# Kernel tuning notes

Measured on AMD Instinct MI355X. Metric: run time of the kernel, lower is better.

## Reference

```python
import jax, jax.numpy as jnp
import numpy as np

IMAGE_SIZE = 256
NEAR = 0.1
FAR = 100.0
CHUNK = 200  # faces per rasterization chunk


def setup_inputs() -> dict:
    key = jax.random.key(0)
    k1, k2, k3 = jax.random.split(key, 3)
    B, Nv, Nf = 1, 10000, 10000
    # vertices sized so that after weak projection (u = f*x + c, f=1015, c=112,
    # orig_size=224) they land inside the image plane; z kept positive.
    xy = jax.random.uniform(k1, (B, Nv, 2), minval=-0.1, maxval=0.1)
    z = jax.random.uniform(k3, (B, Nv, 1), minval=0.4, maxval=0.8)
    vertices = jnp.concatenate([xy, z], axis=-1).astype(jnp.float32)
    faces = jax.random.randint(k2, (B, Nf, 3), 0, Nv).astype(jnp.int64)
    f, c = 1015.0, 112.0
    K = jnp.broadcast_to(jnp.array([[f, 0.0, c], [0.0, f, c], [0.0, 0.0, 1.0]],
                                   dtype=jnp.float32), (B, 3, 3))
    R = jnp.broadcast_to(jnp.eye(3, dtype=jnp.float32), (B, 3, 3))
    t = jnp.zeros((B, 3), dtype=jnp.float32)
    return {"vertices": vertices, "faces": faces, "K": K, "R": R, "t": t,
            "orig_size": 224}


def weak_projection(vertices, K, R, t, orig_size):
    # camera transform: v_cam = v @ R^T + t   [B,N,3]
    v = jnp.einsum('bnj,bkj->bnk', vertices, R) + t[:, None, :]
    x, y, z = v[..., 0], v[..., 1], v[..., 2]
    fx, fy = K[:, 0:1, 0], K[:, 1:2, 1]  # [B,1]
    cx, cy = K[:, 0:1, 2], K[:, 1:2, 2]
    # weak (orthographic-with-focal) projection: no divide by z
    u = fx * x + cx
    w = fy * y + cy
    xn = 2.0 * u / orig_size - 1.0        # NDC x in [-1,1]
    yn = -(2.0 * w / orig_size - 1.0)     # image y down -> NDC y up
    return jnp.stack([xn, yn, z], axis=-1)


def _rasterize_depth(face_verts):
    # face_verts: [B, F, 3, 3] (NDC x, NDC y, camera z)
    B, F = face_verts.shape[0], face_verts.shape[1]
    IS = IMAGE_SIZE
    ps = (2.0 * (jnp.arange(IS, dtype=jnp.float32) + 0.5) / IS) - 1.0
    px = ps[None, :]    # [1, W]
    py = -ps[:, None]   # [H, 1], row 0 is top of image

    def chunk_depth(fc):  # fc: [B, C, 3, 3] -> per-pixel min depth [B, H, W]
        x = fc[..., 0][..., None, None]  # [B,C,3,1,1]
        y = fc[..., 1][..., None, None]
        z = fc[..., 2]                   # [B,C,3]
        dx0, dx1, dx2 = x[:, :, 0] - px, x[:, :, 1] - px, x[:, :, 2] - px  # [B,C,1,W]
        dy0, dy1, dy2 = y[:, :, 0] - py, y[:, :, 1] - py, y[:, :, 2] - py  # [B,C,H,1]
        # edge functions (unnormalized barycentric weights) [B,C,H,W]
        w0 = dx1 * dy2 - dx2 * dy1
        w1 = dx2 * dy0 - dx0 * dy2
        w2 = dx0 * dy1 - dx1 * dy0
        area = w0 + w1 + w2
        s = jnp.sign(area)
        inside = (w0 * s >= 0) & (w1 * s >= 0) & (w2 * s >= 0) & (jnp.abs(area) > 1e-10)
        safe_area = jnp.where(jnp.abs(area) > 1e-10, area, 1.0)
        zp = (w0 * z[:, :, 0, None, None] + w1 * z[:, :, 1, None, None]
              + w2 * z[:, :, 2, None, None]) / safe_area
        valid = inside & (zp > NEAR) & (zp < FAR)
        return jnp.min(jnp.where(valid, zp, FAR), axis=1)  # [B,H,W]

    pad = (-F) % CHUNK
    fv = jnp.pad(face_verts, ((0, 0), (0, pad), (0, 0), (0, 0)))  # degenerate pads -> area 0
    n = (F + pad) // CHUNK
    fv = fv.reshape(B, n, CHUNK, 3, 3).transpose(1, 0, 2, 3, 4)  # [n,B,C,3,3]
    ck = jax.checkpoint(chunk_depth)

    def step(carry, fc):
        return jnp.minimum(carry, ck(fc)), None

    depth0 = jnp.full((B, IS, IS), FAR, dtype=jnp.float32)
    depth, _ = jax.lax.scan(step, depth0, fv)
    return depth


def reference(vertices, faces, K, R, t, orig_size):
    # fill_back: append reversed-winding copies of every face
    faces2 = jnp.concatenate([faces, faces[:, :, ::-1]], axis=1)  # [B,2F,3]
    v = weak_projection(vertices, K, R, t, orig_size)             # [B,Nv,3]
    face_verts = jax.vmap(lambda vb, fb: vb[fb])(v, faces2)       # [B,2F,3,3]
    return _rasterize_depth(face_verts)                           # [B,256,256]
```

## Files before the change

kernel.cpp:

```cpp
#include <hip/hip_runtime.h>

#define IMG 256
#define FARZ 100.0f
#define FARB 0x42C80000u
#define TILE 16
#define NZ 4
#define RND 512
#define BT 512
#define EPS 1e-4f
#define EPSZ 1e-5f
#define DPIX (2.0f / IMG)

typedef float f2 __attribute__((ext_vector_type(2)));
static __device__ __forceinline__ f2 pkfma(f2 a, f2 b, f2 c) {
    return __builtin_elementwise_fma(a, b, c);
}
static __device__ __forceinline__ float wave_max(float v) {
#pragma unroll
    for (int m = 32; m >= 1; m >>= 1) v = fmaxf(v, __shfl_xor(v, m, 64));
    return v;
}
static __device__ __forceinline__ float wave_min(float v) {
#pragma unroll
    for (int m = 32; m >= 1; m >>= 1) v = fminf(v, __shfl_xor(v, m, 64));
    return v;
}

struct Q4 { f2 r0, r1; };
static __device__ __forceinline__ Q4 eval4(float A, float B, float C,
                                           float px0, float py0) {
    Q4 o;
    float w00 = fmaf(B, px0, fmaf(C, py0, A));
    o.r0 = pkfma((f2){B, B}, (f2){0.0f, DPIX}, (f2){w00, w00});
    o.r1 = pkfma((f2){C, C}, (f2){-DPIX, -DPIX}, o.r0);
    return o;
}

__global__ __launch_bounds__(256) void setup(const float* __restrict__ verts,
                                             const int* __restrict__ faces,
                                             const float* __restrict__ K,
                                             const float* __restrict__ Rm,
                                             const float* __restrict__ t,
                                             const int* __restrict__ osz,
                                             float4* __restrict__ Q0,
                                             float4* __restrict__ Q1,
                                             float4* __restrict__ Q2,
                                             float4* __restrict__ BB,
                                             unsigned* __restrict__ gb,
                                             unsigned* __restrict__ out, int Nf) {
    __shared__ float sb[4][4];
    int tid = threadIdx.x;
    int i = blockIdx.x * 256 + tid;
    out[i] = FARB;

    float k0 = 104.0f, k1 = 104.0f, k2 = 104.0f, k3 = 104.0f;
    if (i < Nf) {
        float fx = K[0], cx = K[2], fy = K[4], cy = K[5];
        float os = (float)osz[0];
        float r00 = Rm[0], r01 = Rm[1], r02 = Rm[2];
        float r10 = Rm[3], r11 = Rm[4], r12 = Rm[5];
        float r20 = Rm[6], r21 = Rm[7], r22 = Rm[8];
        float t0 = t[0], t1 = t[1], t2 = t[2];

        float3 p[3];
#pragma unroll
        for (int k = 0; k < 3; ++k) {
            int vi = faces[3 * i + k];
            float vx = verts[3 * vi], vy = verts[3 * vi + 1], vz = verts[3 * vi + 2];
            float x = r00 * vx + r01 * vy + r02 * vz + t0;
            float y = r10 * vx + r11 * vy + r12 * vz + t1;
            float z = r20 * vx + r21 * vy + r22 * vz + t2;
            float u = fx * x + cx;
            float w = fy * y + cy;
            p[k].x = 2.0f * u / os - 1.0f;
            p[k].y = -(2.0f * w / os - 1.0f);
            p[k].z = z;
        }

        float A0 = p[1].x * p[2].y - p[2].x * p[1].y;
        float B0 = p[1].y - p[2].y;
        float C0 = p[2].x - p[1].x;
        float A1 = p[2].x * p[0].y - p[0].x * p[2].y;
        float B1 = p[2].y - p[0].y;
        float C1 = p[0].x - p[2].x;
        float A2 = p[0].x * p[1].y - p[1].x * p[0].y;
        float B2 = p[0].y - p[1].y;
        float C2 = p[1].x - p[0].x;

        float area = A0 + A1 + A2;
        if (fabsf(area) > 1e-10f) {
            float s = (area > 0.0f) ? 1.0f : -1.0f;
            A0 *= s; B0 *= s; C0 *= s;
            A1 *= s; B1 *= s; C1 *= s;
            A2 *= s; B2 *= s; C2 *= s;
            float inv = (1.0f / area) * s;
            float P = (A0 * p[0].z + A1 * p[1].z + A2 * p[2].z) * inv;
            float Q = (B0 * p[0].z + B1 * p[1].z + B2 * p[2].z) * inv;
            float Rr = (C0 * p[0].z + C1 * p[1].z + C2 * p[2].z) * inv;
            Q0[i] = make_float4(A0, B0, C0, A1);
            Q1[i] = make_float4(B1, C1, A2, B2);
            Q2[i] = make_float4(C2, P, Q, Rr);
            float xmn = fminf(p[0].x, fminf(p[1].x, p[2].x));
            float xmx = fmaxf(p[0].x, fmaxf(p[1].x, p[2].x));
            float ymn = fminf(p[0].y, fminf(p[1].y, p[2].y));
            float ymx = fmaxf(p[0].y, fmaxf(p[1].y, p[2].y));
            BB[i] = make_float4(xmn, xmx, ymn, ymx);
            k0 = 4.0f + xmn; k1 = 4.0f - xmx;
            k2 = 4.0f + ymn; k3 = 4.0f - ymx;
        } else {
            Q0[i] = make_float4(0.0f, 0.0f, 0.0f, 0.0f);
            Q1[i] = make_float4(0.0f, 0.0f, 0.0f, 0.0f);
            Q2[i] = make_float4(0.0f, 0.0f, 0.0f, 0.0f);
            BB[i] = make_float4(2.0f, 2.0f, 2.0f, 2.0f);
        }
    }

    k0 = wave_min(k0); k1 = wave_min(k1); k2 = wave_min(k2); k3 = wave_min(k3);
    int wave = tid >> 6, lane = tid & 63;
    if (lane == 0) { sb[wave][0] = k0; sb[wave][1] = k1; sb[wave][2] = k2; sb[wave][3] = k3; }
    __syncthreads();
    if (tid < 4) {
        float v = fminf(fminf(sb[0][tid], sb[1][tid]), fminf(sb[2][tid], sb[3][tid]));
        atomicMin(&gb[tid], __float_as_uint(v));
    }
}

__global__ __launch_bounds__(BT) void raster(const float4* __restrict__ Q0,
                                             const float4* __restrict__ Q1,
                                             const float4* __restrict__ Q2,
                                             const float4* __restrict__ BB,
                                             const unsigned* __restrict__ gb,
                                             unsigned* __restrict__ out,
                                             int Nf, int span) {
    __shared__ float4 sf[RND * 3];
    __shared__ unsigned sdepth[TILE * TILE];
    __shared__ float swr[4];
    __shared__ int scnt;

    const int tid = threadIdx.x;
    const int bx = blockIdx.x, by = blockIdx.y;
    const int wave = tid >> 6, lane = tid & 63;

    const float cx0 = -1.0f + (bx * TILE + 0.5f) * DPIX;
    const float cx1 = cx0 + (TILE - 1) * DPIX;
    const float cyTop = 1.0f - (by * TILE + 0.5f) * DPIX;
    const float cyBot = cyTop - (TILE - 1) * DPIX;
    const float tcx = 0.5f * (cx0 + cx1);
    const float tcy = 0.5f * (cyBot + cyTop);
    const float hx = 0.5f * (cx1 - cx0);
    const float hy = 0.5f * (cyTop - cyBot);

    const float gxmin = __uint_as_float(gb[0]) - 4.0f;
    const float gxmax = 4.0f - __uint_as_float(gb[1]);
    const float gymin = __uint_as_float(gb[2]) - 4.0f;
    const float gymax = 4.0f - __uint_as_float(gb[3]);

    const int col = tid & 15, row = (tid >> 4) & 15;
    const float pxt = cx0 + (float)col * DPIX;
    const float pyt = cyTop - (float)row * DPIX;
    const bool coverable = (pxt >= gxmin - 1e-6f) & (pxt <= gxmax + 1e-6f) &
                           (pyt >= gymin - 1e-6f) & (pyt <= gymax + 1e-6f);
    const int gidx = (by * TILE + row) * IMG + bx * TILE + col;
    unsigned orig = FARB;
    if (tid < 256) {
        orig = out[gidx];
        sdepth[tid] = orig;
    }
    if (tid == 0) scnt = 0;
    __syncthreads();
    float T;
    {
        if (tid < 256) {
            float v = coverable ? __uint_as_float(orig) : 0.0f;
            float wm = wave_max(v);
            if (lane == 0) swr[wave] = wm;
        }
        __syncthreads();
        T = fmaxf(fmaxf(swr[0], swr[1]), fmaxf(swr[2], swr[3]));
    }

    const int qx = (lane & 7) * 2, qy = (lane >> 3) * 2;
    const float fpx0 = cx0 + (float)qx * DPIX;
    const float fpy0 = cyTop - (float)qy * DPIX;
    unsigned dmu[4];
    dmu[0] = sdepth[qy * TILE + qx];
    dmu[1] = sdepth[qy * TILE + qx + 1];
    dmu[2] = sdepth[(qy + 1) * TILE + qx];
    dmu[3] = sdepth[(qy + 1) * TILE + qx + 1];

    const int fbase = blockIdx.z * span;
    const int fend = min(fbase + span, Nf);

    for (int base = fbase; base < fend; base += RND) {
        int f = base + tid;
        if (f < fend) {
            float4 b = BB[f];
            bool keep = (b.x <= cx1 + EPS) & (b.y >= cx0 - EPS) &
                        (b.z <= cyTop + EPS) & (b.w >= cyBot - EPS);
            if (keep) {
                float4 q0 = Q0[f], q1 = Q1[f], q2 = Q2[f];
                float m0 = fmaf(q0.y, tcx, fmaf(q0.z, tcy, q0.x)) +
                           fabsf(q0.y) * hx + fabsf(q0.z) * hy;
                float m1 = fmaf(q1.x, tcx, fmaf(q1.y, tcy, q0.w)) +
                           fabsf(q1.x) * hx + fabsf(q1.y) * hy;
                float m2 = fmaf(q1.w, tcx, fmaf(q2.x, tcy, q1.z)) +
                           fabsf(q1.w) * hx + fabsf(q2.x) * hy;
                float zc = fmaf(q2.z, tcx, fmaf(q2.w, tcy, q2.y));
                float zmn = zc - fabsf(q2.z) * hx - fabsf(q2.w) * hy;
                if ((m0 >= -EPS) & (m1 >= -EPS) & (m2 >= -EPS) &
                    (zmn <= T + EPSZ)) {
                    int slot = atomicAdd(&scnt, 1);
                    sf[3 * slot + 0] = q0;
                    sf[3 * slot + 1] = q1;
                    sf[3 * slot + 2] = q2;
                }
            }
        }
        __syncthreads();
        const int n = scnt;

#pragma unroll 2
        for (int j = wave; j < n; j += 8) {
            float4 c0 = sf[3 * j + 0];
            float4 c1 = sf[3 * j + 1];
            float4 c2 = sf[3 * j + 2];
            Q4 w0 = eval4(c0.x, c0.y, c0.z, fpx0, fpy0);
            Q4 w1 = eval4(c0.w, c1.x, c1.y, fpx0, fpy0);
            Q4 w2 = eval4(c1.z, c1.w, c2.x, fpx0, fpy0);
            Q4 zz = eval4(c2.y, c2.z, c2.w, fpx0, fpy0);
            float s0 = fminf(fminf(w0.r0.x, w1.r0.x), w2.r0.x);
            float s1 = fminf(fminf(w0.r0.y, w1.r0.y), w2.r0.y);
            float s2 = fminf(fminf(w0.r1.x, w1.r1.x), w2.r1.x);
            float s3 = fminf(fminf(w0.r1.y, w1.r1.y), w2.r1.y);
            unsigned u0 = (__float_as_uint(s0) & 0x80000000u) | __float_as_uint(zz.r0.x);
            unsigned u1 = (__float_as_uint(s1) & 0x80000000u) | __float_as_uint(zz.r0.y);
            unsigned u2 = (__float_as_uint(s2) & 0x80000000u) | __float_as_uint(zz.r1.x);
            unsigned u3 = (__float_as_uint(s3) & 0x80000000u) | __float_as_uint(zz.r1.y);
            dmu[0] = min(dmu[0], u0);
            dmu[1] = min(dmu[1], u1);
            dmu[2] = min(dmu[2], u2);
            dmu[3] = min(dmu[3], u3);
        }

        atomicMin(&sdepth[qy * TILE + qx], dmu[0]);
        atomicMin(&sdepth[qy * TILE + qx + 1], dmu[1]);
        atomicMin(&sdepth[(qy + 1) * TILE + qx], dmu[2]);
        atomicMin(&sdepth[(qy + 1) * TILE + qx + 1], dmu[3]);
        __syncthreads();

        if (base + RND < fend) {
            if (tid == 0) scnt = 0;
            if (tid < 256) {
                float v = coverable ? __uint_as_float(sdepth[tid]) : 0.0f;
                float wm = wave_max(v);
                if (lane == 0) swr[wave] = wm;
            }
            __syncthreads();
            T = fmaxf(fmaxf(swr[0], swr[1]), fmaxf(swr[2], swr[3]));
        }
    }

    if (tid < 256) {
        unsigned fv = sdepth[tid];
        if (fv < orig) atomicMin(out + gidx, fv);
    }
}

extern "C" void kernel_launch(void* const* d_in, const int* in_sizes, int n_in,
                              void* d_out, int out_size, void* d_ws, size_t ws_size,
                              hipStream_t stream) {
    const float* verts = (const float*)d_in[0];
    const int* faces   = (const int*)d_in[1];
    const float* K     = (const float*)d_in[2];
    const float* Rm    = (const float*)d_in[3];
    const float* t     = (const float*)d_in[4];
    const int* osz     = (const int*)d_in[5];

    int Nf = in_sizes[1] / 3;
    int span = (Nf + NZ - 1) / NZ;

    float4* ws4 = (float4*)d_ws;
    float4* Q0 = ws4;
    float4* Q1 = ws4 + Nf;
    float4* Q2 = ws4 + 2 * Nf;
    float4* BB = ws4 + 3 * Nf;
    unsigned* gb = (unsigned*)(ws4 + 4 * Nf);
    unsigned* out = (unsigned*)d_out;

    setup<<<(IMG * IMG) / 256, 256, 0, stream>>>(verts, faces, K, Rm, t, osz,
                                                 Q0, Q1, Q2, BB, gb, out, Nf);

    raster<<<dim3(IMG / TILE, IMG / TILE, NZ), BT, 0, stream>>>(
        Q0, Q1, Q2, BB, gb, out, Nf, span);
}
```

Before: 93.77 us.

## Depth-sort faces into buckets and stop rasterizing once tile depth bound is reached

Faces are binned by their minimum depth with a histogram, an exclusive scan and a scatter kernel, then interleaved across the z-split so each raster block walks faces front-to-back. Each block stops once the next face bucket exceeds the current tile's maximum depth, skipping occluded faces. Per-thread shared atomics for compaction are also replaced by wave ballot plus one atomic per wave. This adds three small kernels, a memset and extra workspace traffic, and relies on depth-sorted order for early termination to pay off.

```diff
diff --git a/kernel.cpp b/kernel.cpp
--- a/kernel.cpp
+++ b/kernel.cpp
@@ -10,6 +10,7 @@
 #define EPS 1e-4f
 #define EPSZ 1e-5f
 #define DPIX (2.0f / IMG)
+#define NB 256
 
 typedef float f2 __attribute__((ext_vector_type(2)));
 static __device__ __forceinline__ f2 pkfma(f2 a, f2 b, f2 c) {
@@ -47,6 +48,8 @@
                                              float4* __restrict__ Q2,
                                              float4* __restrict__ BB,
                                              unsigned* __restrict__ gb,
+                                             unsigned* __restrict__ hist,
+                                             int* __restrict__ key,
                                              unsigned* __restrict__ out, int Nf) {
     __shared__ float sb[4][4];
     int tid = threadIdx.x;
@@ -88,6 +91,7 @@
         float C2 = p[1].x - p[0].x;
 
         float area = A0 + A1 + A2;
+        int bkt = NB - 1;
         if (fabsf(area) > 1e-10f) {
             float s = (area > 0.0f) ? 1.0f : -1.0f;
             A0 *= s; B0 *= s; C0 *= s;
@@ -107,12 +111,17 @@
             BB[i] = make_float4(xmn, xmx, ymn, ymx);
             k0 = 4.0f + xmn; k1 = 4.0f - xmx;
             k2 = 4.0f + ymn; k3 = 4.0f - ymx;
+            float minz = fminf(p[0].z, fminf(p[1].z, p[2].z));
+            int b = (int)floorf(minz * (float)NB);
+            bkt = min(max(b, 0), NB - 1);
         } else {
             Q0[i] = make_float4(0.0f, 0.0f, 0.0f, 0.0f);
             Q1[i] = make_float4(0.0f, 0.0f, 0.0f, 0.0f);
             Q2[i] = make_float4(0.0f, 0.0f, 0.0f, 0.0f);
             BB[i] = make_float4(2.0f, 2.0f, 2.0f, 2.0f);
         }
+        key[i] = bkt;
+        atomicAdd(&hist[bkt], 1u);
     }
 
     k0 = wave_min(k0); k1 = wave_min(k1); k2 = wave_min(k2); k3 = wave_min(k3);
@@ -125,20 +134,64 @@
     }
 }
 
+__global__ __launch_bounds__(NB) void scan(const unsigned* __restrict__ hist,
+                                           int* __restrict__ offs,
+                                           int* __restrict__ wbase) {
+    __shared__ int s[NB];
+    int tid = threadIdx.x;
+    int v = (int)hist[tid];
+    s[tid] = v;
+    __syncthreads();
+#pragma unroll
+    for (int d = 1; d < NB; d <<= 1) {
+        int add = (tid >= d) ? s[tid - d] : 0;
+        __syncthreads();
+        s[tid] += add;
+        __syncthreads();
+    }
+    int incl = s[tid];
+    offs[tid + 1] = incl;
+    if (tid == 0) offs[0] = 0;
+    wbase[tid] = incl - v;
+}
+
+__global__ __launch_bounds__(256) void scatter(const float4* __restrict__ Q0,
+                                               const float4* __restrict__ Q1,
+                                               const float4* __restrict__ Q2,
+                                               const float4* __restrict__ BB,
+                                               const int* __restrict__ key,
+                                               int* __restrict__ wbase,
+                                               float4* __restrict__ Qs0,
+                                               float4* __restrict__ Qs1,
+                                               float4* __restrict__ Qs2,
+                                               float4* __restrict__ BBs,
+                                               int Nf, int L) {
+    int i = blockIdx.x * 256 + threadIdx.x;
+    if (i >= Nf) return;
+    int b = key[i];
+    int j = atomicAdd(&wbase[b], 1);
+    int slot = (j & (NZ - 1)) * L + (j >> 2);
+    Qs0[slot] = Q0[i];
+    Qs1[slot] = Q1[i];
+    Qs2[slot] = Q2[i];
+    BBs[slot] = BB[i];
+}
+
 __global__ __launch_bounds__(BT) void raster(const float4* __restrict__ Q0,
                                              const float4* __restrict__ Q1,
                                              const float4* __restrict__ Q2,
                                              const float4* __restrict__ BB,
                                              const unsigned* __restrict__ gb,
+                                             const int* __restrict__ offs,
                                              unsigned* __restrict__ out,
-                                             int Nf, int span) {
+                                             int Nf, int L) {
     __shared__ float4 sf[RND * 3];
     __shared__ unsigned sdepth[TILE * TILE];
     __shared__ float swr[4];
     __shared__ int scnt;
 
     const int tid = threadIdx.x;
-    const int bx = blockIdx.x, by = blockIdx.y;
+    const int bx = blockIdx.x, by = blockIdx.y, bz = blockIdx.z;
     const int wave = tid >> 6, lane = tid & 63;
 
     const float cx0 = -1.0f + (bx * TILE + 0.5f) * DPIX;
@@ -188,17 +241,27 @@
     dmu[2] = sdepth[(qy + 1) * TILE + qx];
     dmu[3] = sdepth[(qy + 1) * TILE + qx + 1];
 
-    const int fbase = blockIdx.z * span;
-    const int fend = min(fbase + span, Nf);
-
-    for (int base = fbase; base < fend; base += RND) {
-        int f = base + tid;
-        if (f < fend) {
-            float4 b = BB[f];
-            bool keep = (b.x <= cx1 + EPS) & (b.y >= cx0 - EPS) &
-                        (b.z <= cyTop + EPS) & (b.w >= cyBot - EPS);
-            if (keep) {
-                float4 q0 = Q0[f], q1 = Q1[f], q2 = Q2[f];
+    const int sbase = bz * L;
+    const int cnt = (Nf - bz + NZ - 1) / NZ;
+
+    int done = 0;
+    for (;;) {
+        int bk = (int)floorf((T + EPSZ) * (float)NB);
+        bk = min(max(bk, 0), NB - 1);
+        int P = offs[bk + 1];
+        int lim = min(cnt, (P + NZ - 1) / NZ);
+        if (done >= lim) break;
+
+        bool keep = false;
+        float4 q0, q1, q2;
+        int fl = done + tid;
+        if (fl < lim) {
+            float4 b = BB[sbase + fl];
+            if ((b.x <= cx1 + EPS) & (b.y >= cx0 - EPS) &
+                (b.z <= cyTop + EPS) & (b.w >= cyBot - EPS)) {
+                q0 = Q0[sbase + fl];
+                q1 = Q1[sbase + fl];
+                q2 = Q2[sbase + fl];
                 float m0 = fmaf(q0.y, tcx, fmaf(q0.z, tcy, q0.x)) +
                            fabsf(q0.y) * hx + fabsf(q0.z) * hy;
                 float m1 = fmaf(q1.x, tcx, fmaf(q1.y, tcy, q0.w)) +
@@ -207,14 +270,22 @@
                            fabsf(q1.w) * hx + fabsf(q2.x) * hy;
                 float zc = fmaf(q2.z, tcx, fmaf(q2.w, tcy, q2.y));
                 float zmn = zc - fabsf(q2.z) * hx - fabsf(q2.w) * hy;
-                if ((m0 >= -EPS) & (m1 >= -EPS) & (m2 >= -EPS) &
-                    (zmn <= T + EPSZ)) {
-                    int slot = atomicAdd(&scnt, 1);
-                    sf[3 * slot + 0] = q0;
-                    sf[3 * slot + 1] = q1;
-                    sf[3 * slot + 2] = q2;
-                }
+                keep = (m0 >= -EPS) & (m1 >= -EPS) & (m2 >= -EPS) &
+                       (zmn <= T + EPSZ);
             }
+        }
+        unsigned long long mk = __ballot(keep);
+        int base_w = 0;
+        if (lane == 0) {
+            int c = __popcll(mk);
+            if (c) base_w = atomicAdd(&scnt, c);
+        }
+        base_w = __shfl(base_w, 0, 64);
+        if (keep) {
+            int slot = base_w + __popcll(mk & ((1ull << lane) - 1ull));
+            sf[3 * slot + 0] = q0;
+            sf[3 * slot + 1] = q1;
+            sf[3 * slot + 2] = q2;
         }
         __syncthreads();
         const int n = scnt;
@@ -248,16 +319,15 @@
         atomicMin(&sdepth[(qy + 1) * TILE + qx + 1], dmu[3]);
         __syncthreads();
 
-        if (base + RND < fend) {
-            if (tid == 0) scnt = 0;
-            if (tid < 256) {
-                float v = coverable ? __uint_as_float(sdepth[tid]) : 0.0f;
-                float wm = wave_max(v);
-                if (lane == 0) swr[wave] = wm;
-            }
-            __syncthreads();
-            T = fmaxf(fmaxf(swr[0], swr[1]), fmaxf(swr[2], swr[3]));
-        }
+        done += RND;
+        if (tid == 0) scnt = 0;
+        if (tid < 256) {
+            float v = coverable ? __uint_as_float(sdepth[tid]) : 0.0f;
+            float wm = wave_max(v);
+            if (lane == 0) swr[wave] = wm;
+        }
+        __syncthreads();
+        T = fmaxf(fmaxf(swr[0], swr[1]), fmaxf(swr[2], swr[3]));
     }
 
     if (tid < 256) {
@@ -277,19 +347,35 @@
     const int* osz     = (const int*)d_in[5];
 
     int Nf = in_sizes[1] / 3;
-    int span = (Nf + NZ - 1) / NZ;
+    int L = (Nf + NZ - 1) / NZ;
 
     float4* ws4 = (float4*)d_ws;
-    float4* Q0 = ws4;
-    float4* Q1 = ws4 + Nf;
-    float4* Q2 = ws4 + 2 * Nf;
-    float4* BB = ws4 + 3 * Nf;
-    unsigned* gb = (unsigned*)(ws4 + 4 * Nf);
+    float4* Q0  = ws4;
+    float4* Q1  = ws4 + Nf;
+    float4* Q2  = ws4 + 2 * Nf;
+    float4* BB  = ws4 + 3 * Nf;
+    float4* Qs0 = ws4 + 4 * Nf;
+    float4* Qs1 = ws4 + 5 * Nf;
+    float4* Qs2 = ws4 + 6 * Nf;
+    float4* BBs = ws4 + 7 * Nf;
+    unsigned* gb   = (unsigned*)(ws4 + 8 * Nf);
+    unsigned* hist = gb + 4;
+    int* offs  = (int*)(hist + NB);
+    int* wbase = offs + (NB + 1);
+    int* key   = wbase + NB;
     unsigned* out = (unsigned*)d_out;
 
+    hipMemsetAsync(hist, 0, NB * sizeof(unsigned), stream);
+
     setup<<<(IMG * IMG) / 256, 256, 0, stream>>>(verts, faces, K, Rm, t, osz,
-                                                 Q0, Q1, Q2, BB, gb, out, Nf);
+                                                 Q0, Q1, Q2, BB, gb, hist, key,
+                                                 out, Nf);
+
+    scan<<<1, NB, 0, stream>>>(hist, offs, wbase);
+
+    scatter<<<(Nf + 255) / 256, 256, 0, stream>>>(Q0, Q1, Q2, BB, key, wbase,
+                                                  Qs0, Qs1, Qs2, BBs, Nf, L);
 
     raster<<<dim3(IMG / TILE, IMG / TILE, NZ), BT, 0, stream>>>(
-        Q0, Q1, Q2, BB, gb, out, Nf, span);
-}
+        Qs0, Qs1, Qs2, BBs, gb, offs, out, Nf, L);
+}
```

Result: slower. 119.2 us (+27.1%).

## Split tile-covering faces into a depth-only list and aggregate binning atomics per wave

Applied to the files above, without the earlier changes.

During binning, each face is now classified as either fully covering the 16x16 tile (all three conservative edge minima are positive) or only partially covering it. Fully covering faces are stored in a separate compact shared list and rasterized with just the depth plane, which skips the three edge evaluations and the sign-bit merge. Per-thread shared atomicAdds are replaced by one ballot/popcount-based atomic per wave, and rounds with no surviving faces skip the raster loops. The partial-face loop also uses packed min. The cost is extra shared memory, a second loop per round and more classification math per face, and coverage for full-cover faces now depends on the FEPS margin.

```diff
diff --git a/kernel.cpp b/kernel.cpp
--- a/kernel.cpp
+++ b/kernel.cpp
@@ -9,11 +9,15 @@
 #define BT 512
 #define EPS 1e-4f
 #define EPSZ 1e-5f
+#define FEPS 1e-6f
 #define DPIX (2.0f / IMG)
 
 typedef float f2 __attribute__((ext_vector_type(2)));
 static __device__ __forceinline__ f2 pkfma(f2 a, f2 b, f2 c) {
     return __builtin_elementwise_fma(a, b, c);
+}
+static __device__ __forceinline__ f2 pkmin(f2 a, f2 b) {
+    return __builtin_elementwise_min(a, b);
 }
 static __device__ __forceinline__ float wave_max(float v) {
 #pragma unroll
@@ -133,9 +137,10 @@
                                              unsigned* __restrict__ out,
                                              int Nf, int span) {
     __shared__ float4 sf[RND * 3];
+    __shared__ float4 sfz[RND];
     __shared__ unsigned sdepth[TILE * TILE];
     __shared__ float swr[4];
-    __shared__ int scnt;
+    __shared__ int scnt, fcnt;
 
     const int tid = threadIdx.x;
     const int bx = blockIdx.x, by = blockIdx.y;
@@ -166,7 +171,7 @@
         orig = out[gidx];
         sdepth[tid] = orig;
     }
-    if (tid == 0) scnt = 0;
+    if (tid == 0) { scnt = 0; fcnt = 0; }
     __syncthreads();
     float T;
     {
@@ -192,32 +197,69 @@
     const int fend = min(fbase + span, Nf);
 
     for (int base = fbase; base < fend; base += RND) {
+        bool kp = false, kf = false;
+        float4 q0, q1, q2;
         int f = base + tid;
         if (f < fend) {
             float4 b = BB[f];
-            bool keep = (b.x <= cx1 + EPS) & (b.y >= cx0 - EPS) &
-                        (b.z <= cyTop + EPS) & (b.w >= cyBot - EPS);
-            if (keep) {
-                float4 q0 = Q0[f], q1 = Q1[f], q2 = Q2[f];
-                float m0 = fmaf(q0.y, tcx, fmaf(q0.z, tcy, q0.x)) +
-                           fabsf(q0.y) * hx + fabsf(q0.z) * hy;
-                float m1 = fmaf(q1.x, tcx, fmaf(q1.y, tcy, q0.w)) +
-                           fabsf(q1.x) * hx + fabsf(q1.y) * hy;
-                float m2 = fmaf(q1.w, tcx, fmaf(q2.x, tcy, q1.z)) +
-                           fabsf(q1.w) * hx + fabsf(q2.x) * hy;
-                float zc = fmaf(q2.z, tcx, fmaf(q2.w, tcy, q2.y));
+            if ((b.x <= cx1 + EPS) & (b.y >= cx0 - EPS) &
+                (b.z <= cyTop + EPS) & (b.w >= cyBot - EPS)) {
+                q0 = Q0[f]; q1 = Q1[f]; q2 = Q2[f];
+                float c0v = fmaf(q0.y, tcx, fmaf(q0.z, tcy, q0.x));
+                float e0  = fabsf(q0.y) * hx + fabsf(q0.z) * hy;
+                float c1v = fmaf(q1.x, tcx, fmaf(q1.y, tcy, q0.w));
+                float e1  = fabsf(q1.x) * hx + fabsf(q1.y) * hy;
+                float c2v = fmaf(q1.w, tcx, fmaf(q2.x, tcy, q1.z));
+                float e2  = fabsf(q1.w) * hx + fabsf(q2.x) * hy;
+                float zc  = fmaf(q2.z, tcx, fmaf(q2.w, tcy, q2.y));
                 float zmn = zc - fabsf(q2.z) * hx - fabsf(q2.w) * hy;
-                if ((m0 >= -EPS) & (m1 >= -EPS) & (m2 >= -EPS) &
-                    (zmn <= T + EPSZ)) {
-                    int slot = atomicAdd(&scnt, 1);
-                    sf[3 * slot + 0] = q0;
-                    sf[3 * slot + 1] = q1;
-                    sf[3 * slot + 2] = q2;
-                }
+                bool ov = (c0v + e0 >= -EPS) & (c1v + e1 >= -EPS) &
+                          (c2v + e2 >= -EPS) & (zmn <= T + EPSZ);
+                kf = ov & (c0v - e0 >= FEPS) & (c1v - e1 >= FEPS) &
+                     (c2v - e2 >= FEPS);
+                kp = ov & !kf;
             }
         }
+        unsigned long long mp = __ballot(kp);
+        unsigned long long mf = __ballot(kf);
+        int bp = 0, bf = 0;
+        if (lane == 0) {
+            int cp = __popcll(mp);
+            if (cp) bp = atomicAdd(&scnt, cp);
+            int cf = __popcll(mf);
+            if (cf) bf = atomicAdd(&fcnt, cf);
+        }
+        bp = __shfl(bp, 0, 64);
+        bf = __shfl(bf, 0, 64);
+        unsigned long long lm = (1ull << lane) - 1ull;
+        if (kp) {
+            int slot = bp + __popcll(mp & lm);
+            sf[3 * slot + 0] = q0;
+            sf[3 * slot + 1] = q1;
+            sf[3 * slot + 2] = q2;
+        }
+        if (kf) {
+            int slot = bf + __popcll(mf & lm);
+            sfz[slot] = make_float4(q2.y, q2.z, q2.w, 0.0f);
+        }
         __syncthreads();
-        const int n = scnt;
+        const int n = scnt, fn = fcnt;
+        const bool more = (base + RND < fend);
+
+        if ((n | fn) == 0) {
+            __syncthreads();
+            continue;
+        }
+
+#pragma unroll 4
+        for (int j = wave; j < fn; j += 8) {
+            float4 cz = sfz[j];
+            Q4 zz = eval4(cz.x, cz.y, cz.z, fpx0, fpy0);
+            dmu[0] = min(dmu[0], __float_as_uint(zz.r0.x));
+            dmu[1] = min(dmu[1], __float_as_uint(zz.r0.y));
+            dmu[2] = min(dmu[2], __float_as_uint(zz.r1.x));
+            dmu[3] = min(dmu[3], __float_as_uint(zz.r1.y));
+        }
 
 #pragma unroll 2
         for (int j = wave; j < n; j += 8) {
@@ -228,14 +270,12 @@
             Q4 w1 = eval4(c0.w, c1.x, c1.y, fpx0, fpy0);
             Q4 w2 = eval4(c1.z, c1.w, c2.x, fpx0, fpy0);
             Q4 zz = eval4(c2.y, c2.z, c2.w, fpx0, fpy0);
-            float s0 = fminf(fminf(w0.r0.x, w1.r0.x), w2.r0.x);
-            float s1 = fminf(fminf(w0.r0.y, w1.r0.y), w2.r0.y);
-            float s2 = fminf(fminf(w0.r1.x, w1.r1.x), w2.r1.x);
-            float s3 = fminf(fminf(w0.r1.y, w1.r1.y), w2.r1.y);
-            unsigned u0 = (__float_as_uint(s0) & 0x80000000u) | __float_as_uint(zz.r0.x);
-            unsigned u1 = (__float_as_uint(s1) & 0x80000000u) | __float_as_uint(zz.r0.y);
-            unsigned u2 = (__float_as_uint(s2) & 0x80000000u) | __float_as_uint(zz.r1.x);
-            unsigned u3 = (__float_as_uint(s3) & 0x80000000u) | __float_as_uint(zz.r1.y);
+            f2 mn0 = pkmin(pkmin(w0.r0, w1.r0), w2.r0);
+            f2 mn1 = pkmin(pkmin(w0.r1, w1.r1), w2.r1);
+            unsigned u0 = (__float_as_uint(mn0.x) & 0x80000000u) | __float_as_uint(zz.r0.x);
+            unsigned u1 = (__float_as_uint(mn0.y) & 0x80000000u) | __float_as_uint(zz.r0.y);
+            unsigned u2 = (__float_as_uint(mn1.x) & 0x80000000u) | __float_as_uint(zz.r1.x);
+            unsigned u3 = (__float_as_uint(mn1.y) & 0x80000000u) | __float_as_uint(zz.r1.y);
             dmu[0] = min(dmu[0], u0);
             dmu[1] = min(dmu[1], u1);
             dmu[2] = min(dmu[2], u2);
@@ -248,8 +288,8 @@
         atomicMin(&sdepth[(qy + 1) * TILE + qx + 1], dmu[3]);
         __syncthreads();
 
-        if (base + RND < fend) {
-            if (tid == 0) scnt = 0;
+        if (more) {
+            if (tid == 0) { scnt = 0; fcnt = 0; }
             if (tid < 256) {
                 float v = coverable ? __uint_as_float(sdepth[tid]) : 0.0f;
                 float wm = wave_max(v);
```

Result: no change. 94.81 us (+1.1%).

## Compact face bins into packed pixel boxes and index lists in raster

Applied to the files above, without the earlier changes.

Setup now stores each face's coefficients interleaved and packs its pixel-space bounding box into one 32-bit word alongside the minimum vertex depth. Raster culls faces with integer box tests and a cheap min-z test in place of per-tile edge-function tests. It compacts only face indices into shared memory using a ballot-based append, and prefetches the next batch's box data. Each wave reads its coefficients from global memory with a uniform index. Tiles with no coverable pixels exit early, the threshold is computed per wave without block barriers, and conservative culling may let more faces through to shading.

```diff
diff --git a/kernel.cpp b/kernel.cpp
--- a/kernel.cpp
+++ b/kernel.cpp
@@ -7,13 +7,16 @@
 #define NZ 4
 #define RND 512
 #define BT 512
-#define EPS 1e-4f
 #define EPSZ 1e-5f
 #define DPIX (2.0f / IMG)
+#define BBZ_EMPTY 0x00FF00FFu
 
 typedef float f2 __attribute__((ext_vector_type(2)));
 static __device__ __forceinline__ f2 pkfma(f2 a, f2 b, f2 c) {
     return __builtin_elementwise_fma(a, b, c);
+}
+static __device__ __forceinline__ f2 pkmin(f2 a, f2 b) {
+    return __builtin_elementwise_min(a, b);
 }
 static __device__ __forceinline__ float wave_max(float v) {
 #pragma unroll
@@ -42,10 +45,8 @@
                                              const float* __restrict__ Rm,
                                              const float* __restrict__ t,
                                              const int* __restrict__ osz,
-                                             float4* __restrict__ Q0,
-                                             float4* __restrict__ Q1,
-                                             float4* __restrict__ Q2,
-                                             float4* __restrict__ BB,
+                                             float4* __restrict__ QQ,
+                                             float2* __restrict__ BBz,
                                              unsigned* __restrict__ gb,
                                              unsigned* __restrict__ out, int Nf) {
     __shared__ float sb[4][4];
@@ -97,21 +98,30 @@
             float P = (A0 * p[0].z + A1 * p[1].z + A2 * p[2].z) * inv;
             float Q = (B0 * p[0].z + B1 * p[1].z + B2 * p[2].z) * inv;
             float Rr = (C0 * p[0].z + C1 * p[1].z + C2 * p[2].z) * inv;
-            Q0[i] = make_float4(A0, B0, C0, A1);
-            Q1[i] = make_float4(B1, C1, A2, B2);
-            Q2[i] = make_float4(C2, P, Q, Rr);
+            QQ[3 * i + 0] = make_float4(A0, B0, C0, A1);
+            QQ[3 * i + 1] = make_float4(B1, C1, A2, B2);
+            QQ[3 * i + 2] = make_float4(C2, P, Q, Rr);
             float xmn = fminf(p[0].x, fminf(p[1].x, p[2].x));
             float xmx = fmaxf(p[0].x, fmaxf(p[1].x, p[2].x));
             float ymn = fminf(p[0].y, fminf(p[1].y, p[2].y));
             float ymx = fmaxf(p[0].y, fmaxf(p[1].y, p[2].y));
-            BB[i] = make_float4(xmn, xmx, ymn, ymx);
+            float zmv = fminf(p[0].z, fminf(p[1].z, p[2].z));
+            int c0 = (int)floorf((xmn + 1.0f) * 128.0f - 0.52f);
+            int c1 = (int)ceilf ((xmx + 1.0f) * 128.0f - 0.48f);
+            int r0 = (int)floorf((1.0f - ymx) * 128.0f - 0.52f);
+            int r1 = (int)ceilf ((1.0f - ymn) * 128.0f - 0.48f);
+            c0 = min(max(c0, 0), 255); c1 = min(max(c1, 0), 255);
+            r0 = min(max(r0, 0), 255); r1 = min(max(r1, 0), 255);
+            unsigned bb = (unsigned)c0 | ((unsigned)c1 << 8) |
+                          ((unsigned)r0 << 16) | ((unsigned)r1 << 24);
+            BBz[i] = make_float2(__uint_as_float(bb), zmv);
             k0 = 4.0f + xmn; k1 = 4.0f - xmx;
             k2 = 4.0f + ymn; k3 = 4.0f - ymx;
         } else {
-            Q0[i] = make_float4(0.0f, 0.0f, 0.0f, 0.0f);
-            Q1[i] = make_float4(0.0f, 0.0f, 0.0f, 0.0f);
-            Q2[i] = make_float4(0.0f, 0.0f, 0.0f, 0.0f);
-            BB[i] = make_float4(2.0f, 2.0f, 2.0f, 2.0f);
+            QQ[3 * i + 0] = make_float4(0.0f, 0.0f, 0.0f, 0.0f);
+            QQ[3 * i + 1] = make_float4(0.0f, 0.0f, 0.0f, 0.0f);
+            QQ[3 * i + 2] = make_float4(0.0f, 0.0f, 0.0f, 0.0f);
+            BBz[i] = make_float2(__uint_as_float(BBZ_EMPTY), 1e9f);
         }
     }
 
@@ -125,30 +135,22 @@
     }
 }
 
-__global__ __launch_bounds__(BT) void raster(const float4* __restrict__ Q0,
-                                             const float4* __restrict__ Q1,
-                                             const float4* __restrict__ Q2,
-                                             const float4* __restrict__ BB,
-                                             const unsigned* __restrict__ gb,
-                                             unsigned* __restrict__ out,
-                                             int Nf, int span) {
-    __shared__ float4 sf[RND * 3];
+__global__ __launch_bounds__(BT, 8) void raster(const float4* __restrict__ QQ,
+                                                const float2* __restrict__ BBz,
+                                                const unsigned* __restrict__ gb,
+                                                unsigned* __restrict__ out,
+                                                int Nf, int span) {
     __shared__ unsigned sdepth[TILE * TILE];
-    __shared__ float swr[4];
-    __shared__ int scnt;
+    __shared__ int sidx[RND];
+    __shared__ int scnt2[2];
 
     const int tid = threadIdx.x;
     const int bx = blockIdx.x, by = blockIdx.y;
     const int wave = tid >> 6, lane = tid & 63;
-
-    const float cx0 = -1.0f + (bx * TILE + 0.5f) * DPIX;
-    const float cx1 = cx0 + (TILE - 1) * DPIX;
-    const float cyTop = 1.0f - (by * TILE + 0.5f) * DPIX;
-    const float cyBot = cyTop - (TILE - 1) * DPIX;
-    const float tcx = 0.5f * (cx0 + cx1);
-    const float tcy = 0.5f * (cyBot + cyTop);
-    const float hx = 0.5f * (cx1 - cx0);
-    const float hy = 0.5f * (cyTop - cyBot);
+    const int tx0 = bx * TILE, ty0 = by * TILE;
+
+    const float cx0 = -1.0f + (tx0 + 0.5f) * DPIX;
+    const float cyTop = 1.0f - (ty0 + 0.5f) * DPIX;
 
     const float gxmin = __uint_as_float(gb[0]) - 4.0f;
     const float gxmax = 4.0f - __uint_as_float(gb[1]);
@@ -156,108 +158,118 @@
     const float gymax = 4.0f - __uint_as_float(gb[3]);
 
     const int col = tid & 15, row = (tid >> 4) & 15;
-    const float pxt = cx0 + (float)col * DPIX;
-    const float pyt = cyTop - (float)row * DPIX;
-    const bool coverable = (pxt >= gxmin - 1e-6f) & (pxt <= gxmax + 1e-6f) &
-                           (pyt >= gymin - 1e-6f) & (pyt <= gymax + 1e-6f);
-    const int gidx = (by * TILE + row) * IMG + bx * TILE + col;
+    const int gidx = (ty0 + row) * IMG + tx0 + col;
     unsigned orig = FARB;
     if (tid < 256) {
         orig = out[gidx];
         sdepth[tid] = orig;
     }
-    if (tid == 0) scnt = 0;
-    __syncthreads();
-    float T;
-    {
-        if (tid < 256) {
-            float v = coverable ? __uint_as_float(orig) : 0.0f;
-            float wm = wave_max(v);
-            if (lane == 0) swr[wave] = wm;
-        }
-        __syncthreads();
-        T = fmaxf(fmaxf(swr[0], swr[1]), fmaxf(swr[2], swr[3]));
-    }
+    if (tid == 0) { scnt2[0] = 0; scnt2[1] = 0; }
 
     const int qx = (lane & 7) * 2, qy = (lane >> 3) * 2;
     const float fpx0 = cx0 + (float)qx * DPIX;
     const float fpy0 = cyTop - (float)qy * DPIX;
+    int cm = 0;
+    {
+        const float x0 = fpx0, x1 = fpx0 + DPIX;
+        const float y0 = fpy0, y1 = fpy0 - DPIX;
+        const bool cx_0 = (x0 >= gxmin - 1e-6f) & (x0 <= gxmax + 1e-6f);
+        const bool cx_1 = (x1 >= gxmin - 1e-6f) & (x1 <= gxmax + 1e-6f);
+        const bool cy_0 = (y0 >= gymin - 1e-6f) & (y0 <= gymax + 1e-6f);
+        const bool cy_1 = (y1 >= gymin - 1e-6f) & (y1 <= gymax + 1e-6f);
+        cm = (cx_0 & cy_0) | ((cx_1 & cy_0) << 1) |
+             ((cx_0 & cy_1) << 2) | ((cx_1 & cy_1) << 3);
+    }
+    __syncthreads();
+
     unsigned dmu[4];
-    dmu[0] = sdepth[qy * TILE + qx];
-    dmu[1] = sdepth[qy * TILE + qx + 1];
-    dmu[2] = sdepth[(qy + 1) * TILE + qx];
-    dmu[3] = sdepth[(qy + 1) * TILE + qx + 1];
+    float T;
+    {
+        uint2 a = *(const uint2*)&sdepth[qy * TILE + qx];
+        uint2 b = *(const uint2*)&sdepth[(qy + 1) * TILE + qx];
+        dmu[0] = a.x; dmu[1] = a.y; dmu[2] = b.x; dmu[3] = b.y;
+        float m = 0.0f;
+        if (cm & 1) m = fmaxf(m, __uint_as_float(a.x));
+        if (cm & 2) m = fmaxf(m, __uint_as_float(a.y));
+        if (cm & 4) m = fmaxf(m, __uint_as_float(b.x));
+        if (cm & 8) m = fmaxf(m, __uint_as_float(b.y));
+        T = wave_max(m);
+    }
+    if (T == 0.0f) return;
 
     const int fbase = blockIdx.z * span;
     const int fend = min(fbase + span, Nf);
 
+    int f = fbase + tid;
+    float2 bz = (f < fend) ? BBz[f]
+                           : make_float2(__uint_as_float(BBZ_EMPTY), 1e9f);
+
+    int p = 0;
     for (int base = fbase; base < fend; base += RND) {
-        int f = base + tid;
-        if (f < fend) {
-            float4 b = BB[f];
-            bool keep = (b.x <= cx1 + EPS) & (b.y >= cx0 - EPS) &
-                        (b.z <= cyTop + EPS) & (b.w >= cyBot - EPS);
-            if (keep) {
-                float4 q0 = Q0[f], q1 = Q1[f], q2 = Q2[f];
-                float m0 = fmaf(q0.y, tcx, fmaf(q0.z, tcy, q0.x)) +
-                           fabsf(q0.y) * hx + fabsf(q0.z) * hy;
-                float m1 = fmaf(q1.x, tcx, fmaf(q1.y, tcy, q0.w)) +
-                           fabsf(q1.x) * hx + fabsf(q1.y) * hy;
-                float m2 = fmaf(q1.w, tcx, fmaf(q2.x, tcy, q1.z)) +
-                           fabsf(q1.w) * hx + fabsf(q2.x) * hy;
-                float zc = fmaf(q2.z, tcx, fmaf(q2.w, tcy, q2.y));
-                float zmn = zc - fabsf(q2.z) * hx - fabsf(q2.w) * hy;
-                if ((m0 >= -EPS) & (m1 >= -EPS) & (m2 >= -EPS) &
-                    (zmn <= T + EPSZ)) {
-                    int slot = atomicAdd(&scnt, 1);
-                    sf[3 * slot + 0] = q0;
-                    sf[3 * slot + 1] = q1;
-                    sf[3 * slot + 2] = q2;
-                }
+        const unsigned bb = __float_as_uint(bz.x);
+        const bool keep = ((int)(bb & 255u) <= tx0 + 15) &
+                          ((int)((bb >> 8) & 255u) >= tx0) &
+                          ((int)((bb >> 16) & 255u) <= ty0 + 15) &
+                          ((int)(bb >> 24) >= ty0) &
+                          (bz.y <= T + EPSZ);
+        const int fn = f + RND;
+        bz = (fn < fend) ? BBz[fn]
+                         : make_float2(__uint_as_float(BBZ_EMPTY), 1e9f);
+
+        unsigned long long mk = __ballot(keep);
+        int bw = 0;
+        if (lane == 0) {
+            int c = __popcll(mk);
+            if (c) bw = atomicAdd(&scnt2[p], c);
+        }
+        bw = __builtin_amdgcn_readfirstlane(bw);
+        if (keep) sidx[bw + __popcll(mk & ((1ull << lane) - 1ull))] = f;
+        __syncthreads();
+        const int n = scnt2[p];
+        if (tid == 0) scnt2[p ^ 1] = 0;
+
+        if (n > 0) {
+#pragma unroll 2
+            for (int j = wave; j < n; j += 8) {
+                int idx = sidx[j];
+                idx = __builtin_amdgcn_readfirstlane(idx);
+                const float4 c0 = QQ[3 * idx + 0];
+                const float4 c1 = QQ[3 * idx + 1];
+                const float4 c2 = QQ[3 * idx + 2];
+                Q4 w0 = eval4(c0.x, c0.y, c0.z, fpx0, fpy0);
+                Q4 w1 = eval4(c0.w, c1.x, c1.y, fpx0, fpy0);
+                Q4 w2 = eval4(c1.z, c1.w, c2.x, fpx0, fpy0);
+                Q4 zz = eval4(c2.y, c2.z, c2.w, fpx0, fpy0);
+                f2 mn0 = pkmin(pkmin(w0.r0, w1.r0), w2.r0);
+                f2 mn1 = pkmin(pkmin(w0.r1, w1.r1), w2.r1);
+                unsigned u0 = (__float_as_uint(mn0.x) & 0x80000000u) | __float_as_uint(zz.r0.x);
+                unsigned u1 = (__float_as_uint(mn0.y) & 0x80000000u) | __float_as_uint(zz.r0.y);
+                unsigned u2 = (__float_as_uint(mn1.x) & 0x80000000u) | __float_as_uint(zz.r1.x);
+                unsigned u3 = (__float_as_uint(mn1.y) & 0x80000000u) | __float_as_uint(zz.r1.y);
+                dmu[0] = min(dmu[0], u0);
+                dmu[1] = min(dmu[1], u1);
+                dmu[2] = min(dmu[2], u2);
+                dmu[3] = min(dmu[3], u3);
             }
+            atomicMin(&sdepth[qy * TILE + qx], dmu[0]);
+            atomicMin(&sdepth[qy * TILE + qx + 1], dmu[1]);
+            atomicMin(&sdepth[(qy + 1) * TILE + qx], dmu[2]);
+            atomicMin(&sdepth[(qy + 1) * TILE + qx + 1], dmu[3]);
         }
         __syncthreads();
-        const int n = scnt;
-
-#pragma unroll 2
-        for (int j = wave; j < n; j += 8) {
-            float4 c0 = sf[3 * j + 0];
-            float4 c1 = sf[3 * j + 1];
-            float4 c2 = sf[3 * j + 2];
-            Q4 w0 = eval4(c0.x, c0.y, c0.z, fpx0, fpy0);
-            Q4 w1 = eval4(c0.w, c1.x, c1.y, fpx0, fpy0);
-            Q4 w2 = eval4(c1.z, c1.w, c2.x, fpx0, fpy0);
-            Q4 zz = eval4(c2.y, c2.z, c2.w, fpx0, fpy0);
-            float s0 = fminf(fminf(w0.r0.x, w1.r0.x), w2.r0.x);
-            float s1 = fminf(fminf(w0.r0.y, w1.r0.y), w2.r0.y);
-            float s2 = fminf(fminf(w0.r1.x, w1.r1.x), w2.r1.x);
-            float s3 = fminf(fminf(w0.r1.y, w1.r1.y), w2.r1.y);
-            unsigned u0 = (__float_as_uint(s0) & 0x80000000u) | __float_as_uint(zz.r0.x);
-            unsigned u1 = (__float_as_uint(s1) & 0x80000000u) | __float_as_uint(zz.r0.y);
-            unsigned u2 = (__float_as_uint(s2) & 0x80000000u) | __float_as_uint(zz.r1.x);
-            unsigned u3 = (__float_as_uint(s3) & 0x80000000u) | __float_as_uint(zz.r1.y);
-            dmu[0] = min(dmu[0], u0);
-            dmu[1] = min(dmu[1], u1);
-            dmu[2] = min(dmu[2], u2);
-            dmu[3] = min(dmu[3], u3);
-        }
-
-        atomicMin(&sdepth[qy * TILE + qx], dmu[0]);
-        atomicMin(&sdepth[qy * TILE + qx + 1], dmu[1]);
-        atomicMin(&sdepth[(qy + 1) * TILE + qx], dmu[2]);
-        atomicMin(&sdepth[(qy + 1) * TILE + qx + 1], dmu[3]);
-        __syncthreads();
-
-        if (base + RND < fend) {
-            if (tid == 0) scnt = 0;
-            if (tid < 256) {
-                float v = coverable ? __uint_as_float(sdepth[tid]) : 0.0f;
-                float wm = wave_max(v);
-                if (lane == 0) swr[wave] = wm;
-            }
-            __syncthreads();
-            T = fmaxf(fmaxf(swr[0], swr[1]), fmaxf(swr[2], swr[3]));
-        }
+
+        if (n > 0) {
+            uint2 a = *(const uint2*)&sdepth[qy * TILE + qx];
+            uint2 b = *(const uint2*)&sdepth[(qy + 1) * TILE + qx];
+            float m = 0.0f;
+            if (cm & 1) m = fmaxf(m, __uint_as_float(a.x));
+            if (cm & 2) m = fmaxf(m, __uint_as_float(a.y));
+            if (cm & 4) m = fmaxf(m, __uint_as_float(b.x));
+            if (cm & 8) m = fmaxf(m, __uint_as_float(b.y));
+            T = wave_max(m);
+        }
+        f = fn;
+        p ^= 1;
     }
 
     if (tid < 256) {
@@ -279,17 +291,14 @@
     int Nf = in_sizes[1] / 3;
     int span = (Nf + NZ - 1) / NZ;
 
-    float4* ws4 = (float4*)d_ws;
-    float4* Q0 = ws4;
-    float4* Q1 = ws4 + Nf;
-    float4* Q2 = ws4 + 2 * Nf;
-    float4* BB = ws4 + 3 * Nf;
-    unsigned* gb = (unsigned*)(ws4 + 4 * Nf);
+    float4* QQ = (float4*)d_ws;
+    float2* BBz = (float2*)(QQ + 3 * Nf);
+    unsigned* gb = (unsigned*)(BBz + Nf);
     unsigned* out = (unsigned*)d_out;
 
     setup<<<(IMG * IMG) / 256, 256, 0, stream>>>(verts, faces, K, Rm, t, osz,
-                                                 Q0, Q1, Q2, BB, gb, out, Nf);
+                                                 QQ, BBz, gb, out, Nf);
 
     raster<<<dim3(IMG / TILE, IMG / TILE, NZ), BT, 0, stream>>>(
-        Q0, Q1, Q2, BB, gb, out, Nf, span);
-}
+        QQ, BBz, gb, out, Nf, span);
+}
```

Result: slower. 119.9 us (+27.9%).
